# Optimization experiments

Measured on AMD Instinct MI355X. Metric: run time of the kernel, lower is better.

## Reference

```python
import jax, jax.numpy as jnp
import numpy as np

TOPK_POS = 16
TOPK_NEG = 16
EPS = 1e-12  # F.normalize default eps


def _l2norm(x):
    # torch.nn.functional.normalize(p=2, dim=1): x / max(||x||_2, eps)
    n = jnp.sqrt(jnp.sum(x * x, axis=1, keepdims=True))
    return x / jnp.maximum(n, EPS)


def setup_inputs() -> dict:
    key = jax.random.key(0)
    k0, k1, k2, k3, k4 = jax.random.split(key, 5)
    B, I, J, C = 32, 1024, 2048, 1024
    f_rad = jax.random.normal(k0, (B, I), dtype=jnp.float32)
    f_histo = jax.random.normal(k1, (B, J), dtype=jnp.float32)
    rad_mask = jax.random.randint(k2, (B,), 0, 2).astype(bool)
    histo_mask = jax.random.randint(k3, (B,), 0, 2).astype(bool)
    # nn.Linear(in_channels*2, out_channels): weight [C, 2*I], bias [C]
    W = jax.random.normal(k4, (C, 2 * I), dtype=jnp.float32) / np.sqrt(2 * I)
    b = jnp.zeros((C,), dtype=jnp.float32)
    token = jnp.zeros((1, C), dtype=jnp.float32)  # missing_modality_token
    return {"f_rad": f_rad, "f_histo": f_histo, "rad_mask": rad_mask,
            "histo_mask": histo_mask, "W": W, "b": b, "token": token}


def reference(f_rad, f_histo, rad_mask, histo_mask, W, b, token):
    r = _l2norm(f_rad)            # [B, I]
    h = _l2norm(f_histo)          # [B, J]
    sim = jnp.einsum('bi,bj->bij', r, h)  # [B, I, J]
    pos_map = jnp.mean(jax.lax.top_k(sim, TOPK_POS)[0], axis=-1)    # [B, I]
    neg_map = jnp.mean(jax.lax.top_k(-sim, TOPK_NEG)[0], axis=-1)   # [B, I]
    # cat([B,1,I],[B,1,I], dim=1).view(B,-1) == concat(pos, neg) along features
    feat = jnp.concatenate([pos_map, neg_map], axis=1)  # [B, 2I]
    emb = feat @ W.T + b                                 # [B, C]
    # modality_flags = ~torch.min(rad_mask, histo_mask)  (bool AND then NOT)
    flags = (~(rad_mask & histo_mask)).astype(emb.dtype)[:, None]  # [B, 1]
    return emb + token * flags
```

## Files before the change

### kernel.cpp

```cpp
#include <hip/hip_runtime.h>
#include <math.h>

#define NB 32
#define NI 1024
#define NJ 2048
#define NC 1024
#define K2 2048

__device__ __forceinline__ void merge16(float* __restrict__ v,
                                        const float* __restrict__ w) {
    float m[16];
#pragma unroll
    for (int i = 0; i < 16; ++i) m[i] = fmaxf(v[i], w[15 - i]);
#pragma unroll
    for (int st = 8; st >= 1; st >>= 1)
#pragma unroll
        for (int i = 0; i < 16; ++i)
            if ((i & st) == 0) {
                float x = m[i], y = m[i + st];
                m[i] = fmaxf(x, y);
                m[i + st] = fminf(x, y);
            }
#pragma unroll
    for (int i = 0; i < 16; ++i) v[i] = m[i];
}

__global__ __launch_bounds__(256)
void prep_kernel(const float* __restrict__ f_rad,
                 const float* __restrict__ f_histo,
                 const unsigned char* __restrict__ rad_mask,
                 const unsigned char* __restrict__ histo_mask,
                 const float* __restrict__ bias,
                 const float* __restrict__ token,
                 float* __restrict__ F,
                 float* __restrict__ out)
{
    __shared__ float listsP[256][16];
    __shared__ float listsN[256][16];
    __shared__ float red[4];

    const int b = blockIdx.x;
    const int t = threadIdx.x;
    const int wave = t >> 6, lane = t & 63;

    float hv[8];
    float ss = 0.f;
#pragma unroll
    for (int i = 0; i < 8; ++i) {
        hv[i] = f_histo[b * NJ + t + i * 256];
        ss += hv[i] * hv[i];
    }
#pragma unroll
    for (int off = 1; off < 64; off <<= 1) ss += __shfl_xor(ss, off, 64);
    if (lane == 0) red[wave] = ss;

    float vp[16], vn[16];
#pragma unroll
    for (int i = 0; i < 8; ++i) { vp[i] = hv[i]; vn[i] = -hv[i]; }
#pragma unroll
    for (int i = 8; i < 16; ++i) { vp[i] = -INFINITY; vn[i] = -INFINITY; }
#pragma unroll
    for (int a = 0; a < 7; ++a)
#pragma unroll
        for (int c = 0; c < 7 - a; ++c) {
            float x = vp[c], y = vp[c + 1];
            vp[c] = fmaxf(x, y); vp[c + 1] = fminf(x, y);
            x = vn[c]; y = vn[c + 1];
            vn[c] = fmaxf(x, y); vn[c + 1] = fminf(x, y);
        }

    __syncthreads();
    const float hnorm = fmaxf(sqrtf(red[0] + red[1] + red[2] + red[3]), 1e-12f);

#pragma unroll
    for (int i = 0; i < 16; ++i) { listsP[t][i] = vp[i]; listsN[t][i] = vn[i]; }
    __syncthreads();

#pragma unroll
    for (int s = 128; s >= 1; s >>= 1) {
        if (t < s) {
            float wp[16], wn[16];
#pragma unroll
            for (int i = 0; i < 16; ++i) { wp[i] = listsP[t + s][i]; wn[i] = listsN[t + s][i]; }
            merge16(vp, wp);
            merge16(vn, wn);
#pragma unroll
            for (int i = 0; i < 16; ++i) { listsP[t][i] = vp[i]; listsN[t][i] = vn[i]; }
        }
        __syncthreads();
    }

    float sumP = 0.f, sumN = 0.f;
#pragma unroll
    for (int i = 0; i < 16; ++i) { sumP += listsP[0][i]; sumN += listsN[0][i]; }
    const float Hpos = sumP / (16.f * hnorm);
    const float Hneg = -sumN / (16.f * hnorm);

    float rv[4];
    float ss2 = 0.f;
#pragma unroll
    for (int i = 0; i < 4; ++i) {
        rv[i] = f_rad[b * NI + t + i * 256];
        ss2 += rv[i] * rv[i];
    }
#pragma unroll
    for (int off = 1; off < 64; off <<= 1) ss2 += __shfl_xor(ss2, off, 64);
    __syncthreads();
    if (lane == 0) red[wave] = ss2;
    __syncthreads();
    const float rnorm = fmaxf(sqrtf(red[0] + red[1] + red[2] + red[3]), 1e-12f);

#pragma unroll
    for (int i = 0; i < 4; ++i) {
        float rn = rv[i] / rnorm;
        float p, q;
        if (rn > 0.f) { p = rn * Hpos;  q = -rn * Hneg; }
        else          { p = rn * Hneg;  q = -rn * Hpos; }
        F[b * K2 + t + i * 256]      = p;
        F[b * K2 + NI + t + i * 256] = q;
    }

    const float flag = (rad_mask[b] != 0 && histo_mask[b] != 0) ? 0.f : 1.f;
#pragma unroll
    for (int i = 0; i < NC / 256; ++i) {
        int c = t + i * 256;
        out[b * NC + c] = bias[c] + token[c] * flag;
    }
}

__global__ __launch_bounds__(256)
void gemm_kernel(const float4* __restrict__ F4,
                 const float* __restrict__ W,
                 float* __restrict__ out)
{
    const int t = threadIdx.x;
    const int wave = t >> 6, lane = t & 63;
    const int c0 = blockIdx.x * 8 + wave * 2;
    const int kb4 = blockIdx.y * 256;

    float acc0[32], acc1[32];
#pragma unroll
    for (int b = 0; b < 32; ++b) { acc0[b] = 0.f; acc1[b] = 0.f; }

    const float4* Wr0 = reinterpret_cast<const float4*>(W + (size_t)c0 * K2) + kb4;
    const float4* Wr1 = reinterpret_cast<const float4*>(W + (size_t)(c0 + 1) * K2) + kb4;

#pragma unroll
    for (int r = 0; r < 4; ++r) {
        const int kk4 = r * 64 + lane;
        float4 w0 = Wr0[kk4];
        float4 w1 = Wr1[kk4];
#pragma unroll
        for (int b = 0; b < 32; ++b) {
            float4 fv = F4[b * 512 + kb4 + kk4];
            acc0[b] = fmaf(fv.x, w0.x, acc0[b]);
            acc0[b] = fmaf(fv.y, w0.y, acc0[b]);
            acc0[b] = fmaf(fv.z, w0.z, acc0[b]);
            acc0[b] = fmaf(fv.w, w0.w, acc0[b]);
            acc1[b] = fmaf(fv.x, w1.x, acc1[b]);
            acc1[b] = fmaf(fv.y, w1.y, acc1[b]);
            acc1[b] = fmaf(fv.z, w1.z, acc1[b]);
            acc1[b] = fmaf(fv.w, w1.w, acc1[b]);
        }
    }

    float z[32];
#pragma unroll
    for (int b = 0; b < 32; ++b) {
        float a0 = acc0[b] + __shfl_xor(acc0[b], 1, 64);
        float a1 = acc1[b] + __shfl_xor(acc1[b], 1, 64);
        z[b] = (lane & 1) ? a1 : a0;
#pragma unroll
        for (int off = 2; off < 64; off <<= 1)
            z[b] += __shfl_xor(z[b], off, 64);
    }
    const int bsel = lane >> 1;
    float myval = 0.f;
#pragma unroll
    for (int b = 0; b < 32; ++b)
        if (bsel == b) myval = z[b];

    atomicAdd(&out[bsel * NC + c0 + (lane & 1)], myval);
}

extern "C" void kernel_launch(void* const* d_in, const int* in_sizes, int n_in,
                              void* d_out, int out_size, void* d_ws, size_t ws_size,
                              hipStream_t stream) {
    const float* f_rad       = (const float*)d_in[0];
    const float* f_histo     = (const float*)d_in[1];
    const unsigned char* rm  = (const unsigned char*)d_in[2];
    const unsigned char* hm  = (const unsigned char*)d_in[3];
    const float* W           = (const float*)d_in[4];
    const float* bias        = (const float*)d_in[5];
    const float* token       = (const float*)d_in[6];
    float* out = (float*)d_out;
    float* F   = (float*)d_ws;

    prep_kernel<<<NB, 256, 0, stream>>>(f_rad, f_histo, rm, hm, bias, token, F, out);
    dim3 grid(128, 2);
    gemm_kernel<<<grid, 256, 0, stream>>>((const float4*)F, W, out);
}
```

Before: 102.8 us.

## Split GEMM K across more blocks and use transpose-reduce shuffle tree

The GEMM grid grows from 2 to 8 K-splits, so each block handles a single float4 column of K per lane and the K loop disappears. The per-batch butterfly reduction (6 shuffles for each of 32 batch values) is replaced by a recursive-halving transpose reduction that needs far fewer shuffles. This adds more atomicAdds on the output in exchange for more parallelism and less reduction overhead.

```diff
diff --git a/kernel.cpp b/kernel.cpp
--- a/kernel.cpp
+++ b/kernel.cpp
@@ -128,59 +128,65 @@
     }
 }
 
-__global__ __launch_bounds__(256)
+__global__ __launch_bounds__(256, 4)
 void gemm_kernel(const float4* __restrict__ F4,
-                 const float* __restrict__ W,
+                 const float4* __restrict__ WF4,
                  float* __restrict__ out)
 {
     const int t = threadIdx.x;
     const int wave = t >> 6, lane = t & 63;
     const int c0 = blockIdx.x * 8 + wave * 2;
-    const int kb4 = blockIdx.y * 256;
+    const int kk4 = blockIdx.y * 64 + lane;
+
+    const float4 w0 = WF4[(size_t)c0 * 512 + kk4];
+    const float4 w1 = WF4[(size_t)(c0 + 1) * 512 + kk4];
 
     float acc0[32], acc1[32];
 #pragma unroll
     for (int b = 0; b < 32; ++b) { acc0[b] = 0.f; acc1[b] = 0.f; }
 
-    const float4* Wr0 = reinterpret_cast<const float4*>(W + (size_t)c0 * K2) + kb4;
-    const float4* Wr1 = reinterpret_cast<const float4*>(W + (size_t)(c0 + 1) * K2) + kb4;
-
-#pragma unroll
-    for (int r = 0; r < 4; ++r) {
-        const int kk4 = r * 64 + lane;
-        float4 w0 = Wr0[kk4];
-        float4 w1 = Wr1[kk4];
-#pragma unroll
-        for (int b = 0; b < 32; ++b) {
-            float4 fv = F4[b * 512 + kb4 + kk4];
-            acc0[b] = fmaf(fv.x, w0.x, acc0[b]);
-            acc0[b] = fmaf(fv.y, w0.y, acc0[b]);
-            acc0[b] = fmaf(fv.z, w0.z, acc0[b]);
-            acc0[b] = fmaf(fv.w, w0.w, acc0[b]);
-            acc1[b] = fmaf(fv.x, w1.x, acc1[b]);
-            acc1[b] = fmaf(fv.y, w1.y, acc1[b]);
-            acc1[b] = fmaf(fv.z, w1.z, acc1[b]);
-            acc1[b] = fmaf(fv.w, w1.w, acc1[b]);
-        }
-    }
-
+#pragma unroll
+    for (int bb = 0; bb < 32; bb += 4) {
+        float4 fv[4];
+#pragma unroll
+        for (int u = 0; u < 4; ++u) fv[u] = F4[(bb + u) * 512 + kk4];
+#pragma unroll
+        for (int u = 0; u < 4; ++u) {
+            const int b = bb + u;
+            acc0[b] = fmaf(fv[u].x, w0.x, acc0[b]);
+            acc0[b] = fmaf(fv[u].y, w0.y, acc0[b]);
+            acc0[b] = fmaf(fv[u].z, w0.z, acc0[b]);
+            acc0[b] = fmaf(fv[u].w, w0.w, acc0[b]);
+            acc1[b] = fmaf(fv[u].x, w1.x, acc1[b]);
+            acc1[b] = fmaf(fv[u].y, w1.y, acc1[b]);
+            acc1[b] = fmaf(fv[u].z, w1.z, acc1[b]);
+            acc1[b] = fmaf(fv[u].w, w1.w, acc1[b]);
+        }
+    }
+
+    const bool odd = lane & 1;
     float z[32];
 #pragma unroll
     for (int b = 0; b < 32; ++b) {
-        float a0 = acc0[b] + __shfl_xor(acc0[b], 1, 64);
-        float a1 = acc1[b] + __shfl_xor(acc1[b], 1, 64);
-        z[b] = (lane & 1) ? a1 : a0;
-#pragma unroll
-        for (int off = 2; off < 64; off <<= 1)
-            z[b] += __shfl_xor(z[b], off, 64);
-    }
-    const int bsel = lane >> 1;
-    float myval = 0.f;
-#pragma unroll
-    for (int b = 0; b < 32; ++b)
-        if (bsel == b) myval = z[b];
-
-    atomicAdd(&out[bsel * NC + c0 + (lane & 1)], myval);
+        float send = odd ? acc0[b] : acc1[b];
+        float recv = __shfl_xor(send, 1, 64);
+        z[b] = (odd ? acc1[b] : acc0[b]) + recv;
+    }
+
+#pragma unroll
+    for (int j = 0; j < 5; ++j) {
+        const int o = 2 << j;
+        const bool hi = (lane & o) != 0;
+        const int n = 32 >> (j + 1);
+#pragma unroll
+        for (int m = 0; m < n; ++m) {
+            float send = hi ? z[2 * m] : z[2 * m + 1];
+            float recv = __shfl_xor(send, o, 64);
+            z[m] = (hi ? z[2 * m + 1] : z[2 * m]) + recv;
+        }
+    }
+
+    atomicAdd(&out[(lane >> 1) * NC + c0 + (lane & 1)], z[0]);
 }
 
 extern "C" void kernel_launch(void* const* d_in, const int* in_sizes, int n_in,
@@ -197,6 +203,6 @@
     float* F   = (float*)d_ws;
 
     prep_kernel<<<NB, 256, 0, stream>>>(f_rad, f_histo, rm, hm, bias, token, F, out);
-    dim3 grid(128, 2);
-    gemm_kernel<<<grid, 256, 0, stream>>>((const float4*)F, W, out);
-}
+    dim3 grid(128, 8);
+    gemm_kernel<<<grid, 256, 0, stream>>>((const float4*)F, (const float4*)W, out);
+}
```

New measurement: 90.74 us. 1.13x faster.
